# Kernel optimization log

Hardware: AMD Instinct MI355X
Metric: run time of the kernel (lower is better)

The kernel has to match this reference:

```python
import jax, jax.numpy as jnp
import numpy as np

IN_C, HID_C, OUT_C = 128, 256, 128
N_NODES, N_EDGES = 50000, 600000


def setup_inputs() -> dict:
    key = jax.random.key(0)
    ks = jax.random.split(key, 8)
    x = jax.random.normal(ks[0], (N_NODES, IN_C), dtype=jnp.float32)
    edge_index = jax.random.randint(ks[1], (2, N_EDGES), 0, N_NODES, dtype=jnp.int64)
    def glorot(k, shape):
        lim = np.sqrt(6.0 / (shape[0] + shape[1])).astype(np.float32)
        return jax.random.uniform(k, shape, dtype=jnp.float32, minval=-lim, maxval=lim)
    # PyG SAGEConv: out = lin_l(mean_aggr) + lin_r(x_root); bias only in lin_l
    W1_l = glorot(ks[2], (IN_C, HID_C)); b1 = jnp.zeros((HID_C,), jnp.float32)
    W1_r = glorot(ks[3], (IN_C, HID_C))
    W2_l = glorot(ks[4], (HID_C, OUT_C)); b2 = jnp.zeros((OUT_C,), jnp.float32)
    W2_r = glorot(ks[5], (HID_C, OUT_C))
    return {"x": x, "edge_index": edge_index, "W1_l": W1_l, "b1": b1, "W1_r": W1_r,
            "W2_l": W2_l, "b2": b2, "W2_r": W2_r}


def _sage_conv(x, src, dst, W_l, b, W_r):
    n = x.shape[0]
    msg = x[src]  # [E, C] gather from source nodes
    agg = jax.ops.segment_sum(msg, dst, num_segments=n)
    cnt = jax.ops.segment_sum(jnp.ones((src.shape[0],), x.dtype), dst, num_segments=n)
    agg = agg / jnp.maximum(cnt, 1.0)[:, None]  # mean aggregation, zero-deg safe
    return agg @ W_l + b + x @ W_r


def reference(x, edge_index, W1_l, b1, W1_r, W2_l, b2, W2_r):
    src, dst = edge_index[0], edge_index[1]
    h = jax.nn.relu(_sage_conv(x, src, dst, W1_l, b1, W1_r))
    return _sage_conv(h, src, dst, W2_l, b2, W2_r)
```

## Files before the change

### kernel.cpp

```cpp
#include <hip/hip_runtime.h>
#include <hip/hip_bf16.h>


#define N_NODES 50000
#define IN_C    128
#define HID_C   256
#define OUT_C   128
#define N_EDGES 600000
#define SLOTS   64

#define PB_FILL 586
#define PB_W1   (PB_FILL + 256)
#define PB_W2   (PB_W1 + 256)
#define PB_X    (PB_W2 + 6250)

typedef __attribute__((ext_vector_type(8))) short short8;
typedef __attribute__((ext_vector_type(4))) float f32x4;
typedef __attribute__((ext_vector_type(2))) float f32x2;

__device__ __forceinline__ float bf2f(short s) {
    union { unsigned u; float f; } c;
    c.u = ((unsigned)(unsigned short)s) << 16;
    return c.f;
}
__device__ __forceinline__ unsigned f2fp8(float v) {
    return (unsigned)__builtin_amdgcn_cvt_pk_fp8_f32(v, v, 0, false) & 0xffu;
}
__device__ __forceinline__ void acc_fp8x4(float* a, unsigned u) {
    f32x2 lo = __builtin_amdgcn_cvt_pk_f32_fp8(u, false);
    f32x2 hi = __builtin_amdgcn_cvt_pk_f32_fp8(u, true);
    a[0] += lo[0]; a[1] += lo[1]; a[2] += hi[0]; a[3] += hi[1];
}

__device__ __forceinline__ void gload16(const void* g, void* l) {
    typedef const __attribute__((address_space(1))) unsigned int* gp_t;
    typedef __attribute__((address_space(3))) unsigned int* lp_t;
    __builtin_amdgcn_global_load_lds((gp_t)g, (lp_t)l, 16, 0, 0);
}

__global__ __launch_bounds__(256) void prep(
    const float* __restrict__ x, __hip_bfloat16* __restrict__ xbf,
    const float* __restrict__ W1l, const float* __restrict__ W1r,
    const float* __restrict__ W2l, const float* __restrict__ W2r,
    __hip_bfloat16* __restrict__ W1t, __hip_bfloat16* __restrict__ W2t,
    const int* __restrict__ srcI, const int* __restrict__ dstI,
    int* __restrict__ cur, int* __restrict__ colp) {
    int b = blockIdx.x;
    if (b < PB_FILL) {
        int base = b * 1024 + threadIdx.x;
        #pragma unroll
        for (int k = 0; k < 4; ++k) {
            int e = base + k * 256;
            if (e < N_EDGES) {
                int d = dstI[e];
                int pos = atomicAdd(&cur[d], 1);
                if (pos < SLOTS) colp[(size_t)d * SLOTS + pos] = srcI[e];
            }
        }
    } else if (b < PB_W1) {
        int reg = b - PB_FILL;
        int half = reg >> 7;
        int t = (reg & 127) * 256 + threadIdx.x;
        int k = t >> 8, n = t & 255;
        const float* src = half ? W1r : W1l;
        W1t[n * 256 + half * 128 + k] = __float2bfloat16(src[t]);
    } else if (b < PB_W2) {
        int reg = b - PB_W1;
        int half = reg >> 7;
        int t = (reg & 127) * 256 + threadIdx.x;
        int k = t >> 7, n = t & 127;
        const float* src = half ? W2r : W2l;
        W2t[(size_t)(half * 128 + n) * 256 + k] = __float2bfloat16(src[t]);
    } else {
        int t = (b - PB_W2) * 256 + threadIdx.x;
        if (t >= N_NODES * 32) return;
        int row = t >> 5, c = (t & 31) * 4;
        float4 v = *(const float4*)(x + (size_t)row * 128 + c);
        __hip_bfloat16* d = xbf + (size_t)row * 128 + c;
        __hip_bfloat162 p0, p1;
        p0.x = __float2bfloat16(v.x); p0.y = __float2bfloat16(v.y);
        p1.x = __float2bfloat16(v.z); p1.y = __float2bfloat16(v.w);
        *(__hip_bfloat162*)d = p0;
        *(__hip_bfloat162*)(d + 2) = p1;
    }
}

__global__ __launch_bounds__(256, 2) void fused_fwd(
    const __hip_bfloat16* __restrict__ xbf,
    const int* __restrict__ deg, const int* __restrict__ colp,
    const __hip_bfloat16* __restrict__ W1t,
    const float* __restrict__ b1,
    const __hip_bfloat16* __restrict__ W2t,
    const float* __restrict__ b2,
    unsigned char* __restrict__ hp,
    float* __restrict__ pre,
    int M) {
    __shared__ char sm[65536];
    __hip_bfloat16* hAB = (__hip_bfloat16*)sm;
    __hip_bfloat16* Bst = (__hip_bfloat16*)(sm + 32768);

    int tid  = threadIdx.x;
    int wave = tid >> 6, lane = tid & 63;
    int mb   = blockIdx.x * 64;
    int sl   = tid & 15;
    int lrow = lane >> 3, pch = lane & 7;

    for (int pass = 0; pass < 4; ++pass) {
        int r = pass * 16 + (tid >> 4);
        int node = mb + r; if (node >= M) node = M - 1;
        int d = deg[node]; if (d > SLOTS) d = SLOTS;
        const int* col = colp + (size_t)node * SLOTS;
        const __hip_bfloat16* base = xbf + sl * 8;
        float a[8];
        #pragma unroll
        for (int c = 0; c < 8; ++c) a[c] = 0.f;

        short8 v0, v1, v2, v3;
        int j = 0;
        if (d >= 4) {
            int s0 = col[0], s1 = col[1], s2 = col[2], s3 = col[3];
            v0 = *(const short8*)(base + (size_t)s0 * 128);
            v1 = *(const short8*)(base + (size_t)s1 * 128);
            v2 = *(const short8*)(base + (size_t)s2 * 128);
            v3 = *(const short8*)(base + (size_t)s3 * 128);
            for (; j + 8 <= d; j += 4) {
                int t0 = col[j + 4], t1 = col[j + 5];
                int t2 = col[j + 6], t3 = col[j + 7];
                short8 w0 = *(const short8*)(base + (size_t)t0 * 128);
                short8 w1 = *(const short8*)(base + (size_t)t1 * 128);
                short8 w2 = *(const short8*)(base + (size_t)t2 * 128);
                short8 w3 = *(const short8*)(base + (size_t)t3 * 128);
                #pragma unroll
                for (int c = 0; c < 8; ++c)
                    a[c] += (bf2f(v0[c]) + bf2f(v1[c])) + (bf2f(v2[c]) + bf2f(v3[c]));
                v0 = w0; v1 = w1; v2 = w2; v3 = w3;
            }
            #pragma unroll
            for (int c = 0; c < 8; ++c)
                a[c] += (bf2f(v0[c]) + bf2f(v1[c])) + (bf2f(v2[c]) + bf2f(v3[c]));
            j += 4;
        }
        int rem = d - j;
        if (rem > 0) {
            int s0 = col[j];
            int s1 = (rem > 1) ? col[j + 1] : s0;
            int s2 = (rem > 2) ? col[j + 2] : s0;
            short8 t0 = *(const short8*)(base + (size_t)s0 * 128);
            short8 t1 = *(const short8*)(base + (size_t)s1 * 128);
            short8 t2 = *(const short8*)(base + (size_t)s2 * 128);
            #pragma unroll
            for (int c = 0; c < 8; ++c) a[c] += bf2f(t0[c]);
            if (rem > 1) {
                #pragma unroll
                for (int c = 0; c < 8; ++c) a[c] += bf2f(t1[c]);
            }
            if (rem > 2) {
                #pragma unroll
                for (int c = 0; c < 8; ++c) a[c] += bf2f(t2[c]);
            }
        }

        float inv = 1.f / (float)max(d, 1);
        short8 q;
        #pragma unroll
        for (int c = 0; c < 8; ++c) {
            union { __hip_bfloat16 b; short s; } cv;
            cv.b = __float2bfloat16(a[c] * inv);
            q[c] = cv.s;
        }
        int pc = (sl & 8) | ((sl & 7) ^ (r & 7));
        *(short8*)&hAB[r * 256 + pc * 8] = q;
        short8 sv = *(const short8*)(xbf + (size_t)node * 128 + sl * 8);
        *(short8*)&hAB[r * 256 + (16 + pc) * 8] = sv;
    }
    __syncthreads();

    f32x4 acc[4][4];
    #pragma unroll
    for (int i = 0; i < 4; ++i)
        #pragma unroll
        for (int j = 0; j < 4; ++j)
            acc[i][j] = (f32x4){0.f, 0.f, 0.f, 0.f};

    for (int kt = 0; kt < 256; kt += 64) {
        #pragma unroll
        for (int t = 0; t < 8; ++t) {
            int g = wave * 8 + t;
            int rloc = g * 8 + lrow;
            int lch  = pch ^ (rloc & 7);
            gload16(W1t + (size_t)rloc * 256 + kt + lch * 8, &Bst[g * 8 * 64]);
        }
        __syncthreads();
        #pragma unroll
        for (int ks = 0; ks < 64; ks += 32) {
            int chunkL = (ks >> 3) + (lane >> 4);
            short8 af[4], bf[4];
            #pragma unroll
            for (int i = 0; i < 4; ++i) {
                int row = i * 16 + (lane & 15);
                af[i] = *(const short8*)&hAB[row * 256 +
                        ((kt >> 3) + (chunkL ^ (row & 7))) * 8];
            }
            #pragma unroll
            for (int j = 0; j < 4; ++j) {
                int brow = wave * 64 + j * 16 + (lane & 15);
                bf[j] = *(const short8*)&Bst[brow * 64 + (chunkL ^ (brow & 7)) * 8];
            }
            #pragma unroll
            for (int i = 0; i < 4; ++i)
                #pragma unroll
                for (int j = 0; j < 4; ++j)
                    acc[i][j] = __builtin_amdgcn_mfma_f32_16x16x32_bf16(
                        af[i], bf[j], acc[i][j], 0, 0, 0);
        }
        __syncthreads();
    }

    int cn[4];
    float bc[4];
    #pragma unroll
    for (int j = 0; j < 4; ++j) {
        cn[j] = wave * 64 + j * 16 + (lane & 15);
        bc[j] = b1[cn[j]];
    }
    #pragma unroll
    for (int i = 0; i < 4; ++i)
        #pragma unroll
        for (int r = 0; r < 4; ++r) {
            int row = i * 16 + (lane >> 4) * 4 + r;
            #pragma unroll
            for (int j = 0; j < 4; ++j) {
                float v = fmaxf(acc[i][j][r] + bc[j], 0.f);
                int c = cn[j] >> 3;
                int pchk = (c & ~7) | ((c & 7) ^ (row & 7));
                union { __hip_bfloat16 b; short s; } cv;
                cv.b = __float2bfloat16(v);
                *(short*)&hAB[row * 256 + pchk * 8 + (cn[j] & 7)] = cv.s;
            }
        }
    __syncthreads();

    #pragma unroll
    for (int i = 0; i < 4; ++i)
        #pragma unroll
        for (int j = 0; j < 4; ++j)
            acc[i][j] = (f32x4){0.f, 0.f, 0.f, 0.f};

    for (int kt = 0; kt < 256; kt += 64) {
        #pragma unroll
        for (int t = 0; t < 8; ++t) {
            int g = wave * 8 + t;
            int rloc = g * 8 + lrow;
            int lch  = pch ^ (rloc & 7);
            gload16(W2t + (size_t)rloc * 256 + kt + lch * 8, &Bst[g * 8 * 64]);
        }
        __syncthreads();
        #pragma unroll
        for (int ks = 0; ks < 64; ks += 32) {
            int chunkL = (ks >> 3) + (lane >> 4);
            short8 af[4], bf[4];
            #pragma unroll
            for (int i = 0; i < 4; ++i) {
                int row = i * 16 + (lane & 15);
                af[i] = *(const short8*)&hAB[row * 256 +
                        ((kt >> 3) + (chunkL ^ (row & 7))) * 8];
            }
            #pragma unroll
            for (int j = 0; j < 4; ++j) {
                int brow = wave * 64 + j * 16 + (lane & 15);
                bf[j] = *(const short8*)&Bst[brow * 64 + (chunkL ^ (brow & 7)) * 8];
            }
            #pragma unroll
            for (int i = 0; i < 4; ++i)
                #pragma unroll
                for (int j = 0; j < 4; ++j)
                    acc[i][j] = __builtin_amdgcn_mfma_f32_16x16x32_bf16(
                        af[i], bf[j], acc[i][j], 0, 0, 0);
        }
        __syncthreads();
    }

    if (wave < 2) {
        #pragma unroll
        for (int i = 0; i < 4; ++i)
            #pragma unroll
            for (int r = 0; r < 4; ++r) {
                int row = mb + i * 16 + (lane >> 4) * 4 + r;
                if (row >= M) continue;
                #pragma unroll
                for (int j = 0; j < 4; ++j)
                    hp[(size_t)row * 128 + cn[j]] = (unsigned char)f2fp8(acc[i][j][r]);
            }
    } else {
        float bc2[4];
        #pragma unroll
        for (int j = 0; j < 4; ++j) bc2[j] = b2[cn[j] - 128];
        #pragma unroll
        for (int i = 0; i < 4; ++i)
            #pragma unroll
            for (int r = 0; r < 4; ++r) {
                int row = mb + i * 16 + (lane >> 4) * 4 + r;
                if (row >= M) continue;
                #pragma unroll
                for (int j = 0; j < 4; ++j)
                    pre[(size_t)row * 128 + cn[j] - 128] = acc[i][j][r] + bc2[j];
            }
    }
}

__global__ __launch_bounds__(256) void aggregate_fp8_final(
    const unsigned char* __restrict__ feat,
    const int* __restrict__ deg, const int* __restrict__ colp,
    float* __restrict__ outp, const float* __restrict__ pre, int nNodes) {
    int node = blockIdx.x * 16 + (threadIdx.x >> 4);
    int sl   = threadIdx.x & 15;
    if (node >= nNodes) return;
    int beg = node * SLOTS;
    int d   = deg[node]; if (d > SLOTS) d = SLOTS;
    const int* col = colp;
    const unsigned char* base = feat + sl * 8;
    float a[8];
    #pragma unroll
    for (int c = 0; c < 8; ++c) a[c] = 0.f;

    uint2 v0, v1, v2, v3;
    int j = 0;
    if (d >= 4) {
        int s0 = col[beg + 0], s1 = col[beg + 1];
        int s2 = col[beg + 2], s3 = col[beg + 3];
        v0 = *(const uint2*)(base + (size_t)s0 * 128);
        v1 = *(const uint2*)(base + (size_t)s1 * 128);
        v2 = *(const uint2*)(base + (size_t)s2 * 128);
        v3 = *(const uint2*)(base + (size_t)s3 * 128);
        for (; j + 8 <= d; j += 4) {
            int t0 = col[beg + j + 4], t1 = col[beg + j + 5];
            int t2 = col[beg + j + 6], t3 = col[beg + j + 7];
            uint2 w0 = *(const uint2*)(base + (size_t)t0 * 128);
            uint2 w1 = *(const uint2*)(base + (size_t)t1 * 128);
            uint2 w2 = *(const uint2*)(base + (size_t)t2 * 128);
            uint2 w3 = *(const uint2*)(base + (size_t)t3 * 128);
            acc_fp8x4(a,     v0.x); acc_fp8x4(a,     v1.x);
            acc_fp8x4(a,     v2.x); acc_fp8x4(a,     v3.x);
            acc_fp8x4(a + 4, v0.y); acc_fp8x4(a + 4, v1.y);
            acc_fp8x4(a + 4, v2.y); acc_fp8x4(a + 4, v3.y);
            v0 = w0; v1 = w1; v2 = w2; v3 = w3;
        }
        acc_fp8x4(a,     v0.x); acc_fp8x4(a,     v1.x);
        acc_fp8x4(a,     v2.x); acc_fp8x4(a,     v3.x);
        acc_fp8x4(a + 4, v0.y); acc_fp8x4(a + 4, v1.y);
        acc_fp8x4(a + 4, v2.y); acc_fp8x4(a + 4, v3.y);
        j += 4;
    }
    for (; j < d; ++j) {
        uint2 v = *(const uint2*)(base + (size_t)col[beg + j] * 128);
        acc_fp8x4(a, v.x);
        acc_fp8x4(a + 4, v.y);
    }

    float inv = 1.f / (float)max(d, 1);
    const float* pp = pre + (size_t)node * 128 + sl * 8;
    float* op = outp + (size_t)node * 128 + sl * 8;
    float4 p0 = *(const float4*)pp;
    float4 p1 = *(const float4*)(pp + 4);
    *(float4*)op       = make_float4(a[0] * inv + p0.x, a[1] * inv + p0.y,
                                     a[2] * inv + p0.z, a[3] * inv + p0.w);
    *(float4*)(op + 4) = make_float4(a[4] * inv + p1.x, a[5] * inv + p1.y,
                                     a[6] * inv + p1.z, a[7] * inv + p1.w);
}

extern "C" void kernel_launch(void* const* d_in, const int* in_sizes, int n_in,
                              void* d_out, int out_size, void* d_ws, size_t ws_size,
                              hipStream_t stream) {
    const float* x    = (const float*)d_in[0];
    const int*   ei   = (const int*)d_in[1];
    const float* W1l  = (const float*)d_in[2];
    const float* b1   = (const float*)d_in[3];
    const float* W1r  = (const float*)d_in[4];
    const float* W2l  = (const float*)d_in[5];
    const float* b2   = (const float*)d_in[6];
    const float* W2r  = (const float*)d_in[7];
    float* out = (float*)d_out;

    const int N = N_NODES;
    const int* srcI = ei;
    const int* dstI = ei + N_EDGES;

    char* w = (char*)d_ws;
    int*            cur     = (int*)(w + 0);
    int*            colp    = (int*)(w + 204800);
    __hip_bfloat16* W1t     = (__hip_bfloat16*)(w + 13004800);
    __hip_bfloat16* W2t     = (__hip_bfloat16*)(w + 13135872);
    __hip_bfloat16* xbf     = (__hip_bfloat16*)(w + 13266944);
    unsigned char*  hp_f8   = (unsigned char*)(w + 26066944);
    float*          pre     = (float*)(w + 32466944);

    hipMemsetAsync(cur, 0, 200000, stream);
    prep<<<PB_X, 256, 0, stream>>>(x, xbf, W1l, W1r, W2l, W2r, W1t, W2t,
                                   srcI, dstI, cur, colp);

    fused_fwd<<<(N + 63) / 64, 256, 0, stream>>>(
        xbf, cur, colp, W1t, b1, W2t, b2, hp_f8, pre, N);

    aggregate_fp8_final<<<(N + 15) / 16, 256, 0, stream>>>(
        hp_f8, cur, colp, out, pre, N);
}
```

Baseline: 197.0 us.

## Load weight fragments directly from global memory instead of staging in LDS

Removes the LDS staging buffer for the W1t/W2t weight tiles and the global_load_lds copies. Each wave now reads its B fragments straight from global memory (expected to hit L2/cache since weights are shared). This halves shared memory use per block and drops the per-tile barriers, and launch bounds are raised to allow 4 blocks per CU for more occupancy. The cost is more global/cache traffic per MFMA step and exposed load latency inside the inner loop. The register budget per thread also shrinks at the higher occupancy target.

After: 196.6 us (median of 2 runs). About the same (-0.2%).

```diff
diff --git a/kernel.cpp b/kernel.cpp
--- a/kernel.cpp
+++ b/kernel.cpp
@@ -30,12 +30,6 @@
     f32x2 lo = __builtin_amdgcn_cvt_pk_f32_fp8(u, false);
     f32x2 hi = __builtin_amdgcn_cvt_pk_f32_fp8(u, true);
     a[0] += lo[0]; a[1] += lo[1]; a[2] += hi[0]; a[3] += hi[1];
-}
-
-__device__ __forceinline__ void gload16(const void* g, void* l) {
-    typedef const __attribute__((address_space(1))) unsigned int* gp_t;
-    typedef __attribute__((address_space(3))) unsigned int* lp_t;
-    __builtin_amdgcn_global_load_lds((gp_t)g, (lp_t)l, 16, 0, 0);
 }
 
 __global__ __launch_bounds__(256) void prep(
@@ -85,7 +79,7 @@
     }
 }
 
-__global__ __launch_bounds__(256, 2) void fused_fwd(
+__global__ __launch_bounds__(256, 4) void fused_fwd(
     const __hip_bfloat16* __restrict__ xbf,
     const int* __restrict__ deg, const int* __restrict__ colp,
     const __hip_bfloat16* __restrict__ W1t,
@@ -95,15 +89,12 @@
     unsigned char* __restrict__ hp,
     float* __restrict__ pre,
     int M) {
-    __shared__ char sm[65536];
-    __hip_bfloat16* hAB = (__hip_bfloat16*)sm;
-    __hip_bfloat16* Bst = (__hip_bfloat16*)(sm + 32768);
+    __shared__ __hip_bfloat16 hAB[64 * 256];
 
     int tid  = threadIdx.x;
     int wave = tid >> 6, lane = tid & 63;
     int mb   = blockIdx.x * 64;
     int sl   = tid & 15;
-    int lrow = lane >> 3, pch = lane & 7;
 
     for (int pass = 0; pass < 4; ++pass) {
         int r = pass * 16 + (tid >> 4);
@@ -184,17 +175,15 @@
 
     for (int kt = 0; kt < 256; kt += 64) {
         #pragma unroll
-        for (int t = 0; t < 8; ++t) {
-            int g = wave * 8 + t;
-            int rloc = g * 8 + lrow;
-            int lch  = pch ^ (rloc & 7);
-            gload16(W1t + (size_t)rloc * 256 + kt + lch * 8, &Bst[g * 8 * 64]);
-        }
-        __syncthreads();
-        #pragma unroll
         for (int ks = 0; ks < 64; ks += 32) {
             int chunkL = (ks >> 3) + (lane >> 4);
             short8 af[4], bf[4];
+            #pragma unroll
+            for (int j = 0; j < 4; ++j) {
+                int brow = wave * 64 + j * 16 + (lane & 15);
+                bf[j] = *(const short8*)(W1t + (size_t)brow * 256 + kt + ks
+                                         + (lane >> 4) * 8);
+            }
             #pragma unroll
             for (int i = 0; i < 4; ++i) {
                 int row = i * 16 + (lane & 15);
@@ -202,19 +191,14 @@
                         ((kt >> 3) + (chunkL ^ (row & 7))) * 8];
             }
             #pragma unroll
-            for (int j = 0; j < 4; ++j) {
-                int brow = wave * 64 + j * 16 + (lane & 15);
-                bf[j] = *(const short8*)&Bst[brow * 64 + (chunkL ^ (brow & 7)) * 8];
-            }
-            #pragma unroll
             for (int i = 0; i < 4; ++i)
                 #pragma unroll
                 for (int j = 0; j < 4; ++j)
                     acc[i][j] = __builtin_amdgcn_mfma_f32_16x16x32_bf16(
                         af[i], bf[j], acc[i][j], 0, 0, 0);
         }
-        __syncthreads();
-    }
+    }
+    __syncthreads();
 
     int cn[4];
     float bc[4];
@@ -248,17 +232,15 @@
 
     for (int kt = 0; kt < 256; kt += 64) {
         #pragma unroll
-        for (int t = 0; t < 8; ++t) {
-            int g = wave * 8 + t;
-            int rloc = g * 8 + lrow;
-            int lch  = pch ^ (rloc & 7);
-            gload16(W2t + (size_t)rloc * 256 + kt + lch * 8, &Bst[g * 8 * 64]);
-        }
-        __syncthreads();
-        #pragma unroll
         for (int ks = 0; ks < 64; ks += 32) {
             int chunkL = (ks >> 3) + (lane >> 4);
             short8 af[4], bf[4];
+            #pragma unroll
+            for (int j = 0; j < 4; ++j) {
+                int brow = wave * 64 + j * 16 + (lane & 15);
+                bf[j] = *(const short8*)(W2t + (size_t)brow * 256 + kt + ks
+                                         + (lane >> 4) * 8);
+            }
             #pragma unroll
             for (int i = 0; i < 4; ++i) {
                 int row = i * 16 + (lane & 15);
@@ -266,18 +248,12 @@
                         ((kt >> 3) + (chunkL ^ (row & 7))) * 8];
             }
             #pragma unroll
-            for (int j = 0; j < 4; ++j) {
-                int brow = wave * 64 + j * 16 + (lane & 15);
-                bf[j] = *(const short8*)&Bst[brow * 64 + (chunkL ^ (brow & 7)) * 8];
-            }
-            #pragma unroll
             for (int i = 0; i < 4; ++i)
                 #pragma unroll
                 for (int j = 0; j < 4; ++j)
                     acc[i][j] = __builtin_amdgcn_mfma_f32_16x16x32_bf16(
                         af[i], bf[j], acc[i][j], 0, 0, 0);
         }
-        __syncthreads();
     }
 
     if (wave < 2) {
```
